# Kernel tuning notes

Hardware: AMD Instinct MI355X
Metric: run time of the kernel (lower is better)

Reference implementation:

```python
import jax, jax.numpy as jnp
import numpy as np


def setup_inputs() -> dict:
    key = jax.random.key(0)
    k1, k2 = jax.random.split(key)
    L = 1_000_000  # 1000x1000 meshgrid, flattened
    B = 256        # number of receiver positions
    mesh_2D = jax.random.uniform(k1, (L, 2), dtype=jnp.float32) * 10.0  # room coords in [0,10)m
    receiver_pos = jax.random.uniform(k2, (B, 3), dtype=jnp.float32) * 10.0
    return {"mesh_2D": mesh_2D, "receiver_pos": receiver_pos}


def reference(mesh_2D, receiver_pos):
    # mesh_2D: [L, 2], receiver_pos: [B, 3]
    X = mesh_2D[:, 0]  # [L]
    Y = mesh_2D[:, 1]  # [L]
    # Brute-force receiver-to-mesh squared distances, [B, L].
    # (sqrt is monotone, so argmin over squared distances == argmin over distances)
    d2 = (X[None, :] - receiver_pos[:, 0:1]) ** 2 + (Y[None, :] - receiver_pos[:, 1:2]) ** 2
    min_index = jnp.argmin(d2, axis=1).astype(jnp.int32)  # [B]
    L = X.shape[0]
    one_hot = jnp.zeros((L, 1), dtype=mesh_2D.dtype)
    one_hot = one_hot.at[min_index, 0].set(1.0)
    # Faithful to the torch loop quirk: at iteration k<B-1 the not-yet-filled
    # entries of min_index are 0, so index 0 is also set to 1 whenever B > 1.
    if receiver_pos.shape[0] > 1:
        one_hot = one_hot.at[0, 0].set(1.0)
    closest_points = jnp.stack([X[min_index], Y[min_index]], axis=1)  # [B, 2]
    input_tensor = jnp.concatenate([X[:, None], Y[:, None], one_hot], axis=1).astype(jnp.float32)  # [L, 3]
    return input_tensor, closest_points, min_index
```

## Files before the change

### kernel.cpp

```cpp
#include <hip/hip_runtime.h>
#include <math.h>


#define G      256
#define GG     (G * G)
#define BMW    (GG / 32)
#define CELLW  (10.0f / (float)G)
#define W2     (CELLW * CELLW)
#define GATE   (0.98f * W2)
#define INVW   ((float)G / 10.0f)
#define CAP    64
#define PBASE  ((int)0xAAAAAAAA)
#define NCHUNK 1024

__device__ __forceinline__ int clampi(int v, int lo, int hi) {
    return min(max(v, lo), hi);
}

__device__ __forceinline__ int cell_of(float x, float y) {
    int cx = clampi((int)(x * INVW), 0, G - 1);
    int cy = clampi((int)(y * INVW), 0, G - 1);
    return cy * G + cx;
}


__global__ void filter_copy_kernel(const float4* __restrict__ mesh4,
                                   float4* __restrict__ out4,
                                   const float* __restrict__ recv,
                                   int* __restrict__ cellcnt,
                                   float4* __restrict__ cellbuf,
                                   int L, int B) {
    __shared__ unsigned sbm[BMW];
    int tt = threadIdx.x;
    for (int i = tt; i < BMW; i += 256) sbm[i] = 0u;
    __syncthreads();
    for (int r = tt; r < B; r += 256) {
        float rx = recv[3 * r + 0];
        float ry = recv[3 * r + 1];
        int cx = clampi((int)(rx * INVW), 0, G - 1);
        int cy = clampi((int)(ry * INVW), 0, G - 1);
        for (int uy = max(cy - 1, 0); uy <= min(cy + 1, G - 1); ++uy)
            for (int ux = max(cx - 1, 0); ux <= min(cx + 1, G - 1); ++ux) {
                int c = uy * G + ux;
                atomicOr(&sbm[c >> 5], 1u << (c & 31));
            }
    }
    __syncthreads();

    const int nt4 = (L + 3) / 4;
    const int stride = gridDim.x * blockDim.x;
    for (int t = blockIdx.x * blockDim.x + tt; t < nt4; t += stride) {
        int p0 = t * 4;

        float xs[4], ys[4];
        if (p0 + 3 < L) {
            float4 a = mesh4[2 * t];
            float4 b = mesh4[2 * t + 1];
            out4[3 * t + 0] = make_float4(a.x, a.y, 0.0f, a.z);
            out4[3 * t + 1] = make_float4(a.w, 0.0f, b.x, b.y);
            out4[3 * t + 2] = make_float4(0.0f, b.z, b.w, 0.0f);
            xs[0] = a.x; ys[0] = a.y; xs[1] = a.z; ys[1] = a.w;
            xs[2] = b.x; ys[2] = b.y; xs[3] = b.z; ys[3] = b.w;
        } else {
            const float2* mesh = (const float2*)mesh4;
            float* out0 = (float*)out4;
            for (int k = 0; k < 4; ++k) {
                int p = p0 + k;
                if (p >= L) { xs[k] = -100.0f; ys[k] = -100.0f; continue; }
                float2 pt = mesh[p];
                out0[3 * (size_t)p + 0] = pt.x;
                out0[3 * (size_t)p + 1] = pt.y;
                out0[3 * (size_t)p + 2] = 0.0f;
                xs[k] = pt.x; ys[k] = pt.y;
            }
        }

        int c[4];
        unsigned w[4];
        #pragma unroll
        for (int k = 0; k < 4; ++k) c[k] = cell_of(xs[k], ys[k]);
        #pragma unroll
        for (int k = 0; k < 4; ++k) w[k] = sbm[c[k] >> 5];

        #pragma unroll
        for (int k = 0; k < 4; ++k) {
            int p = p0 + k;
            if (p >= L) continue;
            if ((w[k] >> (c[k] & 31)) & 1u) {
                int slot = atomicAdd(&cellcnt[c[k]], 1) - PBASE;
                if (slot >= 0 && slot < CAP) {
                    cellbuf[(size_t)c[k] * CAP + slot] =
                        make_float4(xs[k], ys[k], __int_as_float(p), 0.0f);
                }
            }
        }
    }
}

__global__ void argmin_block_kernel(const float2* __restrict__ mesh,
                                    const float* __restrict__ recv,
                                    const int* __restrict__ cellcnt,
                                    const float4* __restrict__ cellbuf,
                                    float* __restrict__ out0,
                                    float* __restrict__ out1,
                                    float* __restrict__ out2,
                                    int L, int B) {
    const int r = blockIdx.x;
    const int t = threadIdx.x;
    if (r >= B) return;

    __shared__ int scell[9];
    __shared__ int scnt[9];
    __shared__ int sbase[10];
    __shared__ int soflow;
    __shared__ float sd[256];
    __shared__ int   si[256];

    float rx = recv[3 * r + 0];
    float ry = recv[3 * r + 1];
    int cx = clampi((int)(rx * INVW), 0, G - 1);
    int cy = clampi((int)(ry * INVW), 0, G - 1);

    if (t == 0) soflow = 0;
    __syncthreads();
    if (t < 9) {
        int ux = cx + (t % 3) - 1;
        int uy = cy + (t / 3) - 1;
        int cell = -1, n = 0;
        if (ux >= 0 && ux < G && uy >= 0 && uy < G) {
            cell = uy * G + ux;
            n = cellcnt[cell] - PBASE;
            if (n < 0 || n > CAP) { atomicOr(&soflow, 1); n = clampi(n, 0, CAP); }
        }
        scell[t] = cell;
        scnt[t] = n;
    }
    __syncthreads();
    if (t == 0) {
        int acc = 0;
        for (int i = 0; i < 9; ++i) { sbase[i] = acc; acc += scnt[i]; }
        sbase[9] = acc;
    }
    __syncthreads();

    int total = sbase[9];
    float bd2 = INFINITY;
    int bidx = 0x7fffffff;
    for (int pos = t; pos < total; pos += 256) {
        int ci = 0;
        while (pos >= sbase[ci + 1]) ++ci;
        float4 e = cellbuf[(size_t)scell[ci] * CAP + (pos - sbase[ci])];
        int pi = __float_as_int(e.z);
        float dx = e.x - rx;
        float dy = e.y - ry;
        float d2 = __fadd_rn(__fmul_rn(dx, dx), __fmul_rn(dy, dy));
        if (d2 < bd2 || (d2 == bd2 && pi < bidx)) { bd2 = d2; bidx = pi; }
    }
    sd[t] = bd2;
    si[t] = bidx;
    __syncthreads();
    for (int s = 128; s > 0; s >>= 1) {
        if (t < s) {
            float d2 = sd[t + s];
            int   i  = si[t + s];
            if (d2 < sd[t] || (d2 == sd[t] && i < si[t])) { sd[t] = d2; si[t] = i; }
        }
        __syncthreads();
    }

    bool ok = (soflow == 0) && (sd[0] < GATE) && (si[0] >= 0) && (si[0] < L);
    if (!ok) {
        bd2 = INFINITY; bidx = 0x7fffffff;
        for (int j = t; j < L; j += 256) {
            float2 p = mesh[j];
            float dx = p.x - rx;
            float dy = p.y - ry;
            float d2 = __fadd_rn(__fmul_rn(dx, dx), __fmul_rn(dy, dy));
            if (d2 < bd2 || (d2 == bd2 && j < bidx)) { bd2 = d2; bidx = j; }
        }
        __syncthreads();
        sd[t] = bd2;
        si[t] = bidx;
        __syncthreads();
        for (int s = 128; s > 0; s >>= 1) {
            if (t < s) {
                float d2 = sd[t + s];
                int   i  = si[t + s];
                if (d2 < sd[t] || (d2 == sd[t] && i < si[t])) { sd[t] = d2; si[t] = i; }
            }
            __syncthreads();
        }
    }

    if (t == 0) {
        int idx = si[0];
        out2[r] = (float)idx;
        float2 p = mesh[idx];
        out1[2 * r + 0] = p.x;
        out1[2 * r + 1] = p.y;
        out0[3 * (size_t)idx + 2] = 1.0f;
        if (r == 0 && B > 1) out0[2] = 1.0f;
    }
}


__global__ void copy_xy_kernel(const float2* __restrict__ mesh,
                               float* __restrict__ out0, int L) {
    int i = blockIdx.x * blockDim.x + threadIdx.x;
    if (i < L) {
        float2 p = mesh[i];
        out0[3 * i + 0] = p.x;
        out0[3 * i + 1] = p.y;
        out0[3 * i + 2] = 0.0f;
    }
}

__global__ void partial_argmin_kernel(const float2* __restrict__ mesh,
                                      const float* __restrict__ recv,
                                      float* __restrict__ pd2,
                                      int* __restrict__ pidx,
                                      int L, int chunk) {
    const int b = threadIdx.x;
    const int c = blockIdx.x;
    const float rx = recv[3 * b + 0];
    const float ry = recv[3 * b + 1];
    int start = c * chunk;
    int end = min(start + chunk, L);

    float best = INFINITY;
    int bidx = 0x7fffffff;
    #pragma unroll 8
    for (int l = start; l < end; ++l) {
        float2 p = mesh[l];
        float dx = p.x - rx;
        float dy = p.y - ry;
        float d2 = __fadd_rn(__fmul_rn(dx, dx), __fmul_rn(dy, dy));
        if (d2 < best) { best = d2; bidx = l; }
    }
    pd2[c * blockDim.x + b] = best;
    pidx[c * blockDim.x + b] = bidx;
}

__global__ void reduce_finalize_kernel(const float2* __restrict__ mesh,
                                       const float* __restrict__ pd2,
                                       const int* __restrict__ pidx,
                                       float* __restrict__ out0,
                                       float* __restrict__ out1,
                                       float* __restrict__ out2,
                                       int B) {
    const int b = blockIdx.x;
    const int t = threadIdx.x;

    float best = INFINITY;
    int bidx = 0x7fffffff;
    for (int c = t; c < NCHUNK; c += blockDim.x) {
        float d2 = pd2[c * B + b];
        int   i  = pidx[c * B + b];
        if (d2 < best || (d2 == best && i < bidx)) { best = d2; bidx = i; }
    }

    __shared__ float sd[256];
    __shared__ int   si[256];
    sd[t] = best;
    si[t] = bidx;
    __syncthreads();
    for (int s = 128; s > 0; s >>= 1) {
        if (t < s) {
            float d2 = sd[t + s];
            int   i  = si[t + s];
            if (d2 < sd[t] || (d2 == sd[t] && i < si[t])) { sd[t] = d2; si[t] = i; }
        }
        __syncthreads();
    }

    if (t == 0) {
        int idx = si[0];
        out2[b] = (float)idx;
        float2 p = mesh[idx];
        out1[2 * b + 0] = p.x;
        out1[2 * b + 1] = p.y;
        out0[3 * (size_t)idx + 2] = 1.0f;
        if (b == 0) out0[2] = 1.0f;
    }
}

extern "C" void kernel_launch(void* const* d_in, const int* in_sizes, int n_in,
                              void* d_out, int out_size, void* d_ws, size_t ws_size,
                              hipStream_t stream) {
    const float* mesh = (const float*)d_in[0];
    const float* recv = (const float*)d_in[1];
    const int L = in_sizes[0] / 2;
    const int B = in_sizes[1] / 3;

    float* out0 = (float*)d_out;
    float* out1 = out0 + (size_t)3 * L;
    float* out2 = out1 + (size_t)2 * B;

    const size_t need = (size_t)GG * sizeof(int)
                      + (size_t)GG * CAP * sizeof(float4);

    if (ws_size >= need && B <= 4096) {
        int* cellcnt    = (int*)d_ws;
        float4* cellbuf = (float4*)((char*)d_ws + (size_t)GG * sizeof(int));

        filter_copy_kernel<<<512, 256, 0, stream>>>(
            (const float4*)mesh, (float4*)out0, recv, cellcnt, cellbuf, L, B);
        argmin_block_kernel<<<B, 256, 0, stream>>>(
            (const float2*)mesh, recv, cellcnt, cellbuf,
            out0, out1, out2, L, B);
    } else {
        float* pd2  = (float*)d_ws;
        int*   pidx = (int*)((char*)d_ws + sizeof(float) * (size_t)NCHUNK * B);
        const int chunk = (L + NCHUNK - 1) / NCHUNK;

        copy_xy_kernel<<<(L + 255) / 256, 256, 0, stream>>>(
            (const float2*)mesh, out0, L);
        partial_argmin_kernel<<<NCHUNK, B, 0, stream>>>(
            (const float2*)mesh, recv, pd2, pidx, L, chunk);
        reduce_finalize_kernel<<<B, 256, 0, stream>>>(
            (const float2*)mesh, pd2, pidx, out0, out1, out2, B);
    }
}
```

Measured before the change: 71.28 us.

## Split bitmap build into its own kernel and flatten the copy-filter launch

```diff
diff --git a/kernel.cpp b/kernel.cpp
--- a/kernel.cpp
+++ b/kernel.cpp
@@ -24,17 +24,12 @@
 }
 
 
-__global__ void filter_copy_kernel(const float4* __restrict__ mesh4,
-                                   float4* __restrict__ out4,
-                                   const float* __restrict__ recv,
-                                   int* __restrict__ cellcnt,
-                                   float4* __restrict__ cellbuf,
-                                   int L, int B) {
-    __shared__ unsigned sbm[BMW];
-    int tt = threadIdx.x;
-    for (int i = tt; i < BMW; i += 256) sbm[i] = 0u;
-    __syncthreads();
-    for (int r = tt; r < B; r += 256) {
+__global__ void prep_bm_kernel(const float* __restrict__ recv,
+                               unsigned* __restrict__ bm, int B) {
+    int t = threadIdx.x;
+    for (int i = t; i < BMW; i += 256) bm[i] = 0u;
+    __syncthreads();
+    for (int r = t; r < B; r += 256) {
         float rx = recv[3 * r + 0];
         float ry = recv[3 * r + 1];
         int cx = clampi((int)(rx * INVW), 0, G - 1);
@@ -42,57 +37,49 @@
         for (int uy = max(cy - 1, 0); uy <= min(cy + 1, G - 1); ++uy)
             for (int ux = max(cx - 1, 0); ux <= min(cx + 1, G - 1); ++ux) {
                 int c = uy * G + ux;
-                atomicOr(&sbm[c >> 5], 1u << (c & 31));
+                atomicOr(&bm[c >> 5], 1u << (c & 31));
             }
     }
-    __syncthreads();
-
-    const int nt4 = (L + 3) / 4;
-    const int stride = gridDim.x * blockDim.x;
-    for (int t = blockIdx.x * blockDim.x + tt; t < nt4; t += stride) {
-        int p0 = t * 4;
-
-        float xs[4], ys[4];
-        if (p0 + 3 < L) {
-            float4 a = mesh4[2 * t];
-            float4 b = mesh4[2 * t + 1];
-            out4[3 * t + 0] = make_float4(a.x, a.y, 0.0f, a.z);
-            out4[3 * t + 1] = make_float4(a.w, 0.0f, b.x, b.y);
-            out4[3 * t + 2] = make_float4(0.0f, b.z, b.w, 0.0f);
-            xs[0] = a.x; ys[0] = a.y; xs[1] = a.z; ys[1] = a.w;
-            xs[2] = b.x; ys[2] = b.y; xs[3] = b.z; ys[3] = b.w;
-        } else {
-            const float2* mesh = (const float2*)mesh4;
-            float* out0 = (float*)out4;
-            for (int k = 0; k < 4; ++k) {
-                int p = p0 + k;
-                if (p >= L) { xs[k] = -100.0f; ys[k] = -100.0f; continue; }
-                float2 pt = mesh[p];
-                out0[3 * (size_t)p + 0] = pt.x;
-                out0[3 * (size_t)p + 1] = pt.y;
-                out0[3 * (size_t)p + 2] = 0.0f;
-                xs[k] = pt.x; ys[k] = pt.y;
-            }
-        }
-
-        int c[4];
-        unsigned w[4];
-        #pragma unroll
-        for (int k = 0; k < 4; ++k) c[k] = cell_of(xs[k], ys[k]);
-        #pragma unroll
-        for (int k = 0; k < 4; ++k) w[k] = sbm[c[k] >> 5];
-
-        #pragma unroll
-        for (int k = 0; k < 4; ++k) {
-            int p = p0 + k;
-            if (p >= L) continue;
-            if ((w[k] >> (c[k] & 31)) & 1u) {
-                int slot = atomicAdd(&cellcnt[c[k]], 1) - PBASE;
-                if (slot >= 0 && slot < CAP) {
-                    cellbuf[(size_t)c[k] * CAP + slot] =
-                        make_float4(xs[k], ys[k], __int_as_float(p), 0.0f);
-                }
-            }
+}
+
+__global__ void copy_filter_kernel(const float4* __restrict__ mesh4,
+                                   float2* __restrict__ out2v,
+                                   const unsigned* __restrict__ bm,
+                                   int* __restrict__ cellcnt,
+                                   float4* __restrict__ cellbuf, int L) {
+    int t = blockIdx.x * blockDim.x + threadIdx.x;
+    int p0 = t * 2;
+    if (p0 >= L) return;
+
+    float xs[2], ys[2];
+    int np;
+    if (p0 + 1 < L) {
+        float4 a = mesh4[t];
+        out2v[3 * t + 0] = make_float2(a.x, a.y);
+        out2v[3 * t + 1] = make_float2(0.0f, a.z);
+        out2v[3 * t + 2] = make_float2(a.w, 0.0f);
+        xs[0] = a.x; ys[0] = a.y; xs[1] = a.z; ys[1] = a.w;
+        np = 2;
+    } else {
+        const float2* mesh = (const float2*)mesh4;
+        float2 pt = mesh[p0];
+        float* o = (float*)out2v;
+        o[3 * (size_t)p0 + 0] = pt.x;
+        o[3 * (size_t)p0 + 1] = pt.y;
+        o[3 * (size_t)p0 + 2] = 0.0f;
+        xs[0] = pt.x; ys[0] = pt.y;
+        np = 1;
+    }
+
+    #pragma unroll
+    for (int k = 0; k < 2; ++k) {
+        if (k >= np) continue;
+        int c = cell_of(xs[k], ys[k]);
+        if (!((bm[c >> 5] >> (c & 31)) & 1u)) continue;
+        int slot = atomicAdd(&cellcnt[c], 1) - PBASE;
+        if (slot >= 0 && slot < CAP) {
+            cellbuf[(size_t)c * CAP + slot] =
+                make_float4(xs[k], ys[k], __int_as_float(p0 + k), 0.0f);
         }
     }
 }
@@ -296,15 +283,20 @@
     float* out1 = out0 + (size_t)3 * L;
     float* out2 = out1 + (size_t)2 * B;
 
-    const size_t need = (size_t)GG * sizeof(int)
+    const size_t need = (size_t)BMW * sizeof(unsigned)
+                      + (size_t)GG * sizeof(int)
                       + (size_t)GG * CAP * sizeof(float4);
 
     if (ws_size >= need && B <= 4096) {
-        int* cellcnt    = (int*)d_ws;
-        float4* cellbuf = (float4*)((char*)d_ws + (size_t)GG * sizeof(int));
-
-        filter_copy_kernel<<<512, 256, 0, stream>>>(
-            (const float4*)mesh, (float4*)out0, recv, cellcnt, cellbuf, L, B);
+        unsigned* bm    = (unsigned*)d_ws;
+        int* cellcnt    = (int*)(bm + BMW);
+        float4* cellbuf = (float4*)(cellcnt + GG);
+
+        const int nt2 = (L + 1) / 2;
+
+        prep_bm_kernel<<<1, 256, 0, stream>>>(recv, bm, B);
+        copy_filter_kernel<<<(nt2 + 255) / 256, 256, 0, stream>>>(
+            (const float4*)mesh, (float2*)out0, bm, cellcnt, cellbuf, L);
         argmin_block_kernel<<<B, 256, 0, stream>>>(
             (const float2*)mesh, recv, cellcnt, cellbuf,
             out0, out1, out2, L, B);
```

Measured after the change: 74.51 us. 4.5% more time.
